# Optimization experiments

Measured on AMD Instinct MI355X. Metric: run time of the kernel, lower is better.

Reference implementation:

```python
import jax, jax.numpy as jnp
import numpy as np

R = 4096          # proposals per image
D = 4096          # fc7 feature dim (VGG16)
C = 20            # foreground classes (VOC); logits have C+1 with background
IMG_W, IMG_H = 1216.0, 800.0
SCORE_THRESH = 0.05
NMS_THRESH = 0.5
TOPK = 100


def setup_inputs() -> dict:
    key = jax.random.key(0)
    k1, k2, k3, k4, k5 = jax.random.split(key, 5)
    x = jax.random.normal(k1, (R, D), dtype=jnp.float32)
    # build valid xyxy boxes inside the image
    xy = jax.random.uniform(k2, (R, 2)) * jnp.array([IMG_W * 0.8, IMG_H * 0.8])
    wh = jax.random.uniform(k3, (R, 2)) * jnp.array([IMG_W * 0.4, IMG_H * 0.4]) + 8.0
    boxes = jnp.concatenate([xy, xy + wh], axis=1).astype(jnp.float32)
    W_cls = (jax.random.normal(k4, (D, C + 1)) * 0.01).astype(jnp.float32)
    W_det = (jax.random.normal(k5, (D, C + 1)) * 0.01).astype(jnp.float32)
    b_cls = jnp.zeros((C + 1,), jnp.float32)
    b_det = jnp.zeros((C + 1,), jnp.float32)
    return {"x": x, "boxes": boxes, "W_cls": W_cls, "b_cls": b_cls,
            "W_det": W_det, "b_det": b_det}


def _iou_matrix(b):
    # b: (R, 4) xyxy -> (R, R) IoU
    area = (b[:, 2] - b[:, 0]) * (b[:, 3] - b[:, 1])
    lt = jnp.maximum(b[:, None, :2], b[None, :, :2])
    rb = jnp.minimum(b[:, None, 2:], b[None, :, 2:])
    wh = jnp.clip(rb - lt, 0.0)
    inter = wh[..., 0] * wh[..., 1]
    return inter / (area[:, None] + area[None, :] - inter + 1e-9)


def _nms_per_class(sc, iou):
    # sc: (R,) scores for one class; iou: (R, R) shared IoU matrix.
    # Sequential greedy NMS over score-descending order; returns bool keep mask.
    n = sc.shape[0]
    order = jnp.argsort(-sc)

    def step(supp, oi):
        kept = (sc[oi] > SCORE_THRESH) & jnp.logical_not(supp[oi])
        supp = jnp.where(kept, supp | (iou[oi] > NMS_THRESH), supp)
        return supp, kept

    _, keep_sorted = jax.lax.scan(step, jnp.zeros((n,), bool), order)
    return jnp.zeros((n,), bool).at[order].set(keep_sorted)


def reference(x, boxes, W_cls, b_cls, W_det, b_det):
    # WSDDN two-stream head: class softmax x proposal softmax
    cls_logits = x @ W_cls + b_cls                      # (R, C+1)
    det_logits = x @ W_det + b_det                      # (R, C+1)
    scores = jax.nn.softmax(cls_logits, axis=1) * jax.nn.softmax(det_logits, axis=0)
    scores = scores[:, :-1]                             # drop background column (R, C)

    # clip boxes to image (Boxes.clip)
    b = jnp.stack([jnp.clip(boxes[:, 0], 0.0, IMG_W),
                   jnp.clip(boxes[:, 1], 0.0, IMG_H),
                   jnp.clip(boxes[:, 2], 0.0, IMG_W),
                   jnp.clip(boxes[:, 3], 0.0, IMG_H)], axis=1)

    iou = _iou_matrix(b)                                # (R, R)
    # per-class NMS (batched_nms with class-agnostic boxes == independent per-class NMS)
    keep = jax.vmap(lambda s: _nms_per_class(s, iou), in_axes=1, out_axes=1)(scores)  # (R, C)

    kept_scores = scores * keep.astype(scores.dtype)
    flat = kept_scores.reshape(-1)                      # (R*C,)
    top_vals, top_idx = jax.lax.top_k(flat, TOPK)
    top_prop = top_idx // C
    top_cls = top_idx % C
    top_boxes = b[top_prop]                             # (TOPK, 4)
    return top_vals, top_boxes, top_cls
```

## Files before the change

kernel.cpp:

```cpp
#include <hip/hip_runtime.h>
#include <math.h>

#define R_N 4096
#define D_N 4096
#define C_N 20
#define IMG_W_F 1216.0f
#define IMG_H_F 800.0f
#define SCORE_TH 0.05f
#define NMS_TH 0.5f
#define TOPK_N 100

#define WF_WORDS   (128 * 2 * 64 * 4)
#define DET_OFF    (WF_WORDS)
#define DET_WORDS  (R_N * 24)
#define CTRL_OFF   (DET_OFF + DET_WORDS)
#define CAND_R_OFF (CTRL_OFF + 64)
#define CAND_D_OFF (CAND_R_OFF + 640)
#define CAND_S_OFF (CAND_D_OFF + 640)

typedef short bf16x8 __attribute__((ext_vector_type(8)));
typedef float f32x4  __attribute__((ext_vector_type(4)));

__device__ __forceinline__ unsigned pk(float a, float b) {
  return __builtin_amdgcn_perm(__float_as_uint(a), __float_as_uint(b), 0x07060302u);
}
__device__ __forceinline__ float fexp(float x) { return __expf(x); }

__global__ __launch_bounds__(256) void wT_kernel(
    const float* __restrict__ Wd, uint4* __restrict__ Wfrag,
    float* __restrict__ ctrl) {
  const int e = blockIdx.x * 256 + threadIdx.x;
  const int l = e & 63;
  const int ct = (e >> 6) & 1;
  const int gs = e >> 7;
  const int c = ct * 16 + (l & 15);
  const int k0 = gs * 32 + (l >> 4) * 8;
  float w[8];
  if (c < 21) {
#pragma unroll
    for (int j = 0; j < 8; j++) w[j] = Wd[(size_t)(k0 + j) * 21 + c];
  } else {
#pragma unroll
    for (int j = 0; j < 8; j++) w[j] = 0.f;
  }
  uint4 v;
  v.x = pk(w[1], w[0]); v.y = pk(w[3], w[2]);
  v.z = pk(w[5], w[4]); v.w = pk(w[7], w[6]);
  Wfrag[(gs * 2 + ct) * 64 + l] = v;
  if (e < 64) ctrl[e] = 0.f;
}

__global__ __launch_bounds__(1024) void detgemm_kernel(
    const float* __restrict__ x, const uint4* __restrict__ Wfrag,
    float* __restrict__ detlog, float* __restrict__ dsum) {
  __shared__ float red[16 * 512];
  const int t = threadIdx.x;
  const int w = t >> 6, l = t & 63;
  const int r16 = l & 15, q = l >> 4;
  const int r0 = blockIdx.x * 16;

  const float* xrow = x + (size_t)(r0 + r16) * D_N + w * 256 + q * 8;

  float4 a[16];
#pragma unroll
  for (int s = 0; s < 8; s++) {
    a[2 * s]     = *(const float4*)(xrow + s * 32);
    a[2 * s + 1] = *(const float4*)(xrow + s * 32 + 4);
  }

  f32x4 acc0 = {0.f, 0.f, 0.f, 0.f};
  f32x4 acc1 = {0.f, 0.f, 0.f, 0.f};
#pragma unroll
  for (int s = 0; s < 8; s++) {
    const int gs = w * 8 + s;
    union { uint4 u; bf16x8 v; } b0, b1;
    b0.u = Wfrag[(gs * 2 + 0) * 64 + l];
    b1.u = Wfrag[(gs * 2 + 1) * 64 + l];
    union { bf16x8 v; unsigned u[4]; } af;
    af.u[0] = pk(a[2 * s].y,     a[2 * s].x);
    af.u[1] = pk(a[2 * s].w,     a[2 * s].z);
    af.u[2] = pk(a[2 * s + 1].y, a[2 * s + 1].x);
    af.u[3] = pk(a[2 * s + 1].w, a[2 * s + 1].z);
    acc0 = __builtin_amdgcn_mfma_f32_16x16x32_bf16(af.v, b0.v, acc0, 0, 0, 0);
    acc1 = __builtin_amdgcn_mfma_f32_16x16x32_bf16(af.v, b1.v, acc1, 0, 0, 0);
  }

  *(f32x4*)(&red[w * 512 + (0  + r16) * 16 + q * 4]) = acc0;
  *(f32x4*)(&red[w * 512 + (16 + r16) * 16 + q * 4]) = acc1;
  __syncthreads();
  if (t < 512) {
    float v = 0.f;
#pragma unroll
    for (int w2 = 0; w2 < 16; w2++) v += red[w2 * 512 + t];
    red[t] = v;
  }
  __syncthreads();
  if (t < 21) {
    float s = 0.f;
#pragma unroll
    for (int r = 0; r < 16; r++) {
      float v = red[t * 16 + r];
      detlog[(size_t)(r0 + r) * 24 + t] = v;
      s += fexp(v);
    }
    atomicAdd(&dsum[t], s);
  }
}

__device__ __forceinline__ void load_clip_box(const float* boxes, int r, float* b) {
  b[0] = fminf(fmaxf(boxes[r * 4 + 0], 0.f), IMG_W_F);
  b[1] = fminf(fmaxf(boxes[r * 4 + 1], 0.f), IMG_H_F);
  b[2] = fminf(fmaxf(boxes[r * 4 + 2], 0.f), IMG_W_F);
  b[3] = fminf(fmaxf(boxes[r * 4 + 3], 0.f), IMG_H_F);
}

__global__ __launch_bounds__(256) void finish_kernel(
    const float* __restrict__ x, const float* __restrict__ Wc,
    const float* __restrict__ b_cls, const float* __restrict__ detlog,
    const float* __restrict__ dsum, int* __restrict__ nc, int* __restrict__ done,
    int* __restrict__ cand_r, float* __restrict__ cand_d, float* __restrict__ cand_s,
    const float* __restrict__ boxes, float* __restrict__ out) {
  __shared__ float sd[20];
  __shared__ bool s_last;
  const int t = threadIdx.x;
  if (t < 20) sd[t] = dsum[t];
  __syncthreads();

  const int r = blockIdx.x * 256 + t;
  for (int c = 0; c < 20; c++) {
    float dsm = fexp(detlog[(size_t)r * 24 + c]) / sd[c];
    if (dsm > SCORE_TH) {
      int p = atomicAdd(&nc[c], 1);
      if (p < 32) { cand_r[c * 32 + p] = r; cand_d[c * 32 + p] = dsm; }
    }
  }
  __threadfence();
  __syncthreads();
  if (t == 0) s_last = (atomicAdd(done, 1) == 15);
  __syncthreads();
  if (!s_last) return;
  __threadfence();

  for (int slot = t; slot < 640; slot += 256) {
    const int c = slot >> 5, i = slot & 31;
    int n = nc[c]; if (n > 32) n = 32;
    if (i < n) {
      const int rr = cand_r[slot];
      float lg[21];
#pragma unroll
      for (int j = 0; j < 21; j++) lg[j] = b_cls[j];
      const float* xr = x + (size_t)rr * D_N;
      for (int k = 0; k < D_N; k++) {
        float xv = xr[k];
        const float* wr = Wc + (size_t)k * 21;
#pragma unroll
        for (int j = 0; j < 21; j++) lg[j] = fmaf(xv, wr[j], lg[j]);
      }
      float m = -1e30f;
#pragma unroll
      for (int j = 0; j < 21; j++) m = fmaxf(m, lg[j]);
      float s = 0.f;
#pragma unroll
      for (int j = 0; j < 21; j++) s += fexp(lg[j] - m);
      float p = fexp(lg[c] - m) / s;
      cand_s[slot] = p * cand_d[slot];
    }
  }
  __syncthreads();

  __shared__ int   s_kc;
  __shared__ int   s_ki[512];
  __shared__ float s_ks[512];
  __shared__ float sval[TOPK_N];
  __shared__ int   sidx[TOPK_N];
  if (t == 0) s_kc = 0;
  if (t < TOPK_N) { sval[t] = 0.f; sidx[t] = 0; }
  __syncthreads();

  if (t < 20) {
    const int c = t;
    int n = nc[c]; if (n > 32) n = 32;
    float s[32]; int rr[32]; int n2 = 0;
    for (int i = 0; i < n; i++) {
      float sc = cand_s[c * 32 + i];
      if (sc > SCORE_TH) { s[n2] = sc; rr[n2] = cand_r[c * 32 + i]; n2++; }
    }
    for (int i = 1; i < n2; i++) {
      float si = s[i]; int ri = rr[i];
      int j = i - 1;
      while (j >= 0 && (s[j] < si || (s[j] == si && rr[j] > ri))) {
        s[j + 1] = s[j]; rr[j + 1] = rr[j]; j--;
      }
      s[j + 1] = si; rr[j + 1] = ri;
    }
    unsigned supp = 0;
    for (int i = 0; i < n2; i++) {
      if (supp & (1u << i)) continue;
      int g = atomicAdd(&s_kc, 1);
      if (g < 512) { s_ki[g] = rr[i] * C_N + c; s_ks[g] = s[i]; }
      float bi[4]; load_clip_box(boxes, rr[i], bi);
      float ai = (bi[2] - bi[0]) * (bi[3] - bi[1]);
      for (int j = i + 1; j < n2; j++) {
        if (supp & (1u << j)) continue;
        float bj[4]; load_clip_box(boxes, rr[j], bj);
        float aj = (bj[2] - bj[0]) * (bj[3] - bj[1]);
        float lx = fmaxf(bi[0], bj[0]), ly = fmaxf(bi[1], bj[1]);
        float rx = fminf(bi[2], bj[2]), ry = fminf(bi[3], bj[3]);
        float wdt = fmaxf(rx - lx, 0.f), hgt = fmaxf(ry - ly, 0.f);
        float inter = wdt * hgt;
        float iou = inter / (ai + aj - inter + 1e-9f);
        if (iou > NMS_TH) supp |= (1u << j);
      }
    }
  }
  __syncthreads();

  int m = s_kc; if (m > 512) m = 512;
  for (int i = t; i < m; i += 256) {
    float si = s_ks[i]; int xi = s_ki[i];
    int rank = 0;
    for (int j = 0; j < m; j++) {
      float sj = s_ks[j]; int xj = s_ki[j];
      if (sj > si || (sj == si && xj < xi)) rank++;
    }
    if (rank < TOPK_N) { sval[rank] = si; sidx[rank] = xi; }
  }
  __syncthreads();
  if (t == 0) {
    int f = m < TOPK_N ? m : TOPK_N;
    int cur = 0;
    for (int slot = f; slot < TOPK_N; slot++) {
      for (;;) {
        bool member = false;
        for (int j = 0; j < m; j++)
          if (s_ki[j] == cur) { member = true; break; }
        if (!member) break;
        cur++;
      }
      sval[slot] = 0.f;
      sidx[slot] = cur;
      cur++;
    }
  }
  __syncthreads();
  if (t < TOPK_N) {
    int idx = sidx[t];
    int prop = idx / C_N;
    int cls = idx - prop * C_N;
    float b[4]; load_clip_box(boxes, prop, b);
    out[t] = sval[t];
    out[TOPK_N + t * 4 + 0] = b[0];
    out[TOPK_N + t * 4 + 1] = b[1];
    out[TOPK_N + t * 4 + 2] = b[2];
    out[TOPK_N + t * 4 + 3] = b[3];
    out[TOPK_N * 5 + t] = (float)cls;
  }
}

extern "C" void kernel_launch(void* const* d_in, const int* in_sizes, int n_in,
                              void* d_out, int out_size, void* d_ws, size_t ws_size,
                              hipStream_t stream) {
  const float* x     = (const float*)d_in[0];
  const float* boxes = (const float*)d_in[1];
  const float* W_cls = (const float*)d_in[2];
  const float* b_cls = (const float*)d_in[3];
  const float* W_det = (const float*)d_in[4];

  float* out = (float*)d_out;
  float* ws = (float*)d_ws;
  uint4* Wfrag    = (uint4*)ws;
  float* detlog   = ws + DET_OFF;
  float* dsum     = ws + CTRL_OFF;
  int*   nc       = (int*)(ws + CTRL_OFF) + 24;
  int*   done     = (int*)(ws + CTRL_OFF) + 44;
  int*   cand_r   = (int*)(ws + CAND_R_OFF);
  float* cand_d   = ws + CAND_D_OFF;
  float* cand_s   = ws + CAND_S_OFF;

  wT_kernel     <<<64,  256,  0, stream>>>(W_det, Wfrag, dsum);
  detgemm_kernel<<<256, 1024, 0, stream>>>(x, Wfrag, detlog, dsum);
  finish_kernel <<<16,  256,  0, stream>>>(x, W_cls, b_cls, detlog, dsum,
                                           nc, done, cand_r, cand_d, cand_s,
                                           boxes, out);
}
```

Measured before the change: 122.3 us.

## Fuse weight prep, det GEMM and finish into one kernel with last-block tail

```diff
diff --git a/kernel.cpp b/kernel.cpp
--- a/kernel.cpp
+++ b/kernel.cpp
@@ -10,57 +10,37 @@
 #define NMS_TH 0.5f
 #define TOPK_N 100
 
-#define WF_WORDS   (128 * 2 * 64 * 4)
-#define DET_OFF    (WF_WORDS)
-#define DET_WORDS  (R_N * 24)
-#define CTRL_OFF   (DET_OFF + DET_WORDS)
-#define CAND_R_OFF (CTRL_OFF + 64)
-#define CAND_D_OFF (CAND_R_OFF + 640)
-#define CAND_S_OFF (CAND_D_OFF + 640)
-
 typedef short bf16x8 __attribute__((ext_vector_type(8)));
 typedef float f32x4  __attribute__((ext_vector_type(4)));
+
+__device__ int g_done;
 
 __device__ __forceinline__ unsigned pk(float a, float b) {
   return __builtin_amdgcn_perm(__float_as_uint(a), __float_as_uint(b), 0x07060302u);
 }
 __device__ __forceinline__ float fexp(float x) { return __expf(x); }
 
-__global__ __launch_bounds__(256) void wT_kernel(
-    const float* __restrict__ Wd, uint4* __restrict__ Wfrag,
-    float* __restrict__ ctrl) {
-  const int e = blockIdx.x * 256 + threadIdx.x;
-  const int l = e & 63;
-  const int ct = (e >> 6) & 1;
-  const int gs = e >> 7;
-  const int c = ct * 16 + (l & 15);
-  const int k0 = gs * 32 + (l >> 4) * 8;
-  float w[8];
-  if (c < 21) {
-#pragma unroll
-    for (int j = 0; j < 8; j++) w[j] = Wd[(size_t)(k0 + j) * 21 + c];
-  } else {
-#pragma unroll
-    for (int j = 0; j < 8; j++) w[j] = 0.f;
-  }
-  uint4 v;
-  v.x = pk(w[1], w[0]); v.y = pk(w[3], w[2]);
-  v.z = pk(w[5], w[4]); v.w = pk(w[7], w[6]);
-  Wfrag[(gs * 2 + ct) * 64 + l] = v;
-  if (e < 64) ctrl[e] = 0.f;
+__device__ __forceinline__ void load_clip_box(const float* boxes, int r, float* b) {
+  b[0] = fminf(fmaxf(boxes[r * 4 + 0], 0.f), IMG_W_F);
+  b[1] = fminf(fmaxf(boxes[r * 4 + 1], 0.f), IMG_H_F);
+  b[2] = fminf(fmaxf(boxes[r * 4 + 2], 0.f), IMG_W_F);
+  b[3] = fminf(fmaxf(boxes[r * 4 + 3], 0.f), IMG_H_F);
 }
 
-__global__ __launch_bounds__(1024) void detgemm_kernel(
-    const float* __restrict__ x, const uint4* __restrict__ Wfrag,
-    float* __restrict__ detlog, float* __restrict__ dsum) {
-  __shared__ float red[16 * 512];
+__global__ __launch_bounds__(1024) void fused_kernel(
+    const float* __restrict__ x, const float* __restrict__ Wd,
+    const float* __restrict__ Wc, const float* __restrict__ b_cls,
+    const float* __restrict__ boxes,
+    float* __restrict__ detlog, float* __restrict__ out) {
+  __shared__ float smem[10752];
+  __shared__ int s_lastf;
+
   const int t = threadIdx.x;
   const int w = t >> 6, l = t & 63;
   const int r16 = l & 15, q = l >> 4;
   const int r0 = blockIdx.x * 16;
 
   const float* xrow = x + (size_t)(r0 + r16) * D_N + w * 256 + q * 8;
-
   float4 a[16];
 #pragma unroll
   for (int s = 0; s < 8; s++) {
@@ -68,15 +48,36 @@
     a[2 * s + 1] = *(const float4*)(xrow + s * 32 + 4);
   }
 
+  float* wb = smem + w * 672;
+  const int c0  = l & 15;
+  const bool v1 = (c0 < 5);
+  const int cc1 = v1 ? (16 + c0) : 0;
+  const int rb  = q * 8;
+
   f32x4 acc0 = {0.f, 0.f, 0.f, 0.f};
   f32x4 acc1 = {0.f, 0.f, 0.f, 0.f};
 #pragma unroll
   for (int s = 0; s < 8; s++) {
-    const int gs = w * 8 + s;
-    union { uint4 u; bf16x8 v; } b0, b1;
-    b0.u = Wfrag[(gs * 2 + 0) * 64 + l];
-    b1.u = Wfrag[(gs * 2 + 1) * 64 + l];
-    union { bf16x8 v; unsigned u[4]; } af;
+    const float* p = Wd + (size_t)((w * 256 + s * 32) * 21);
+    float4 w0 = *(const float4*)(p + 4 * l);
+    float4 w1 = *(const float4*)(p + 4 * l + 256);
+    *(float4*)(wb + 4 * l)       = w0;
+    *(float4*)(wb + 4 * l + 256) = w1;
+    if (l < 40) {
+      float4 w2 = *(const float4*)(p + 4 * l + 512);
+      *(float4*)(wb + 4 * l + 512) = w2;
+    }
+    union { bf16x8 v; unsigned u[4]; } b0, b1, af;
+#pragma unroll
+    for (int jj = 0; jj < 4; jj++) {
+      float e0 = wb[(rb + 2 * jj)     * 21 + c0];
+      float e1 = wb[(rb + 2 * jj + 1) * 21 + c0];
+      b0.u[jj] = pk(e1, e0);
+      float f0 = wb[(rb + 2 * jj)     * 21 + cc1];
+      float f1 = wb[(rb + 2 * jj + 1) * 21 + cc1];
+      unsigned uu = pk(f1, f0);
+      b1.u[jj] = v1 ? uu : 0u;
+    }
     af.u[0] = pk(a[2 * s].y,     a[2 * s].x);
     af.u[1] = pk(a[2 * s].w,     a[2 * s].z);
     af.u[2] = pk(a[2 * s + 1].y, a[2 * s + 1].x);
@@ -85,6 +86,8 @@
     acc1 = __builtin_amdgcn_mfma_f32_16x16x32_bf16(af.v, b1.v, acc1, 0, 0, 0);
   }
 
+  __syncthreads();
+  float* red = smem;
   *(f32x4*)(&red[w * 512 + (0  + r16) * 16 + q * 4]) = acc0;
   *(f32x4*)(&red[w * 512 + (16 + r16) * 16 + q * 4]) = acc1;
   __syncthreads();
@@ -96,54 +99,89 @@
   }
   __syncthreads();
   if (t < 21) {
-    float s = 0.f;
-#pragma unroll
-    for (int r = 0; r < 16; r++) {
-      float v = red[t * 16 + r];
-      detlog[(size_t)(r0 + r) * 24 + t] = v;
-      s += fexp(v);
-    }
-    atomicAdd(&dsum[t], s);
-  }
-}
-
-__device__ __forceinline__ void load_clip_box(const float* boxes, int r, float* b) {
-  b[0] = fminf(fmaxf(boxes[r * 4 + 0], 0.f), IMG_W_F);
-  b[1] = fminf(fmaxf(boxes[r * 4 + 1], 0.f), IMG_H_F);
-  b[2] = fminf(fmaxf(boxes[r * 4 + 2], 0.f), IMG_W_F);
-  b[3] = fminf(fmaxf(boxes[r * 4 + 3], 0.f), IMG_H_F);
-}
-
-__global__ __launch_bounds__(256) void finish_kernel(
-    const float* __restrict__ x, const float* __restrict__ Wc,
-    const float* __restrict__ b_cls, const float* __restrict__ detlog,
-    const float* __restrict__ dsum, int* __restrict__ nc, int* __restrict__ done,
-    int* __restrict__ cand_r, float* __restrict__ cand_d, float* __restrict__ cand_s,
-    const float* __restrict__ boxes, float* __restrict__ out) {
-  __shared__ float sd[20];
-  __shared__ bool s_last;
-  const int t = threadIdx.x;
-  if (t < 20) sd[t] = dsum[t];
-  __syncthreads();
-
-  const int r = blockIdx.x * 256 + t;
+#pragma unroll
+    for (int r = 0; r < 16; r++)
+      detlog[(size_t)(r0 + r) * 24 + t] = red[t * 16 + r];
+  }
+
+  __threadfence();
+  __syncthreads();
+  if (t == 0) s_lastf = (atomicAdd(&g_done, 1) == 255) ? 1 : 0;
+  __syncthreads();
+  if (!s_lastf) return;
+  __threadfence();
+
+  float* sd     = smem;
+  int*   nc_l   = (int*)(smem + 32);
+  int*   cand_r = (int*)(smem + 64);
+  float* cand_d = smem + 704;
+  float* cand_s = smem + 1344;
+  int*   s_ki   = (int*)(smem + 1984);
+  float* s_ks   = smem + 2496;
+  float* sval   = smem + 3008;
+  int*   sidx   = (int*)(smem + 3108);
+  float* wred   = smem + 3208;
+  int*   s_kc   = (int*)(smem + 3528);
+
+  float ps[20];
+#pragma unroll
+  for (int c = 0; c < 20; c++) ps[c] = 0.f;
+  for (int rr = t; rr < R_N; rr += 1024) {
+    const float* dp = detlog + (size_t)rr * 24;
+    union { float4 v[5]; float f[20]; } u;
+    u.v[0] = *(const float4*)(dp + 0);
+    u.v[1] = *(const float4*)(dp + 4);
+    u.v[2] = *(const float4*)(dp + 8);
+    u.v[3] = *(const float4*)(dp + 12);
+    u.v[4] = *(const float4*)(dp + 16);
+#pragma unroll
+    for (int c = 0; c < 20; c++) ps[c] += fexp(u.f[c]);
+  }
+#pragma unroll
   for (int c = 0; c < 20; c++) {
-    float dsm = fexp(detlog[(size_t)r * 24 + c]) / sd[c];
-    if (dsm > SCORE_TH) {
-      int p = atomicAdd(&nc[c], 1);
-      if (p < 32) { cand_r[c * 32 + p] = r; cand_d[c * 32 + p] = dsm; }
-    }
-  }
-  __threadfence();
-  __syncthreads();
-  if (t == 0) s_last = (atomicAdd(done, 1) == 15);
-  __syncthreads();
-  if (!s_last) return;
-  __threadfence();
-
-  for (int slot = t; slot < 640; slot += 256) {
+    float v = ps[c];
+#pragma unroll
+    for (int off = 32; off; off >>= 1) v += __shfl_xor(v, off, 64);
+    ps[c] = v;
+  }
+  if (l == 0) {
+#pragma unroll
+    for (int c = 0; c < 20; c++) wred[w * 20 + c] = ps[c];
+  }
+  __syncthreads();
+  if (t < 20) {
+    float v = 0.f;
+#pragma unroll
+    for (int w2 = 0; w2 < 16; w2++) v += wred[w2 * 20 + t];
+    sd[t] = v;
+    nc_l[t] = 0;
+  }
+  if (t == 0) *s_kc = 0;
+  if (t < TOPK_N) { sval[t] = 0.f; sidx[t] = 0; }
+  __syncthreads();
+
+  for (int rr = t; rr < R_N; rr += 1024) {
+    const float* dp = detlog + (size_t)rr * 24;
+    union { float4 v[5]; float f[20]; } u;
+    u.v[0] = *(const float4*)(dp + 0);
+    u.v[1] = *(const float4*)(dp + 4);
+    u.v[2] = *(const float4*)(dp + 8);
+    u.v[3] = *(const float4*)(dp + 12);
+    u.v[4] = *(const float4*)(dp + 16);
+#pragma unroll
+    for (int c = 0; c < 20; c++) {
+      float dsm = fexp(u.f[c]) / sd[c];
+      if (dsm > SCORE_TH) {
+        int p = atomicAdd(&nc_l[c], 1);
+        if (p < 32) { cand_r[c * 32 + p] = rr; cand_d[c * 32 + p] = dsm; }
+      }
+    }
+  }
+  __syncthreads();
+
+  for (int slot = t; slot < 640; slot += 1024) {
     const int c = slot >> 5, i = slot & 31;
-    int n = nc[c]; if (n > 32) n = 32;
+    int n = nc_l[c]; if (n > 32) n = 32;
     if (i < n) {
       const int rr = cand_r[slot];
       float lg[21];
@@ -168,18 +206,9 @@
   }
   __syncthreads();
 
-  __shared__ int   s_kc;
-  __shared__ int   s_ki[512];
-  __shared__ float s_ks[512];
-  __shared__ float sval[TOPK_N];
-  __shared__ int   sidx[TOPK_N];
-  if (t == 0) s_kc = 0;
-  if (t < TOPK_N) { sval[t] = 0.f; sidx[t] = 0; }
-  __syncthreads();
-
   if (t < 20) {
     const int c = t;
-    int n = nc[c]; if (n > 32) n = 32;
+    int n = nc_l[c]; if (n > 32) n = 32;
     float s[32]; int rr[32]; int n2 = 0;
     for (int i = 0; i < n; i++) {
       float sc = cand_s[c * 32 + i];
@@ -196,7 +225,7 @@
     unsigned supp = 0;
     for (int i = 0; i < n2; i++) {
       if (supp & (1u << i)) continue;
-      int g = atomicAdd(&s_kc, 1);
+      int g = atomicAdd(s_kc, 1);
       if (g < 512) { s_ki[g] = rr[i] * C_N + c; s_ks[g] = s[i]; }
       float bi[4]; load_clip_box(boxes, rr[i], bi);
       float ai = (bi[2] - bi[0]) * (bi[3] - bi[1]);
@@ -215,8 +244,8 @@
   }
   __syncthreads();
 
-  int m = s_kc; if (m > 512) m = 512;
-  for (int i = t; i < m; i += 256) {
+  int m = *s_kc; if (m > 512) m = 512;
+  for (int i = t; i < m; i += 1024) {
     float si = s_ks[i]; int xi = s_ki[i];
     int rank = 0;
     for (int j = 0; j < m; j++) {
@@ -255,6 +284,7 @@
     out[TOPK_N + t * 4 + 3] = b[3];
     out[TOPK_N * 5 + t] = (float)cls;
   }
+  if (t == 0) g_done = 0;
 }
 
 extern "C" void kernel_launch(void* const* d_in, const int* in_sizes, int n_in,
@@ -266,20 +296,8 @@
   const float* b_cls = (const float*)d_in[3];
   const float* W_det = (const float*)d_in[4];
 
-  float* out = (float*)d_out;
-  float* ws = (float*)d_ws;
-  uint4* Wfrag    = (uint4*)ws;
-  float* detlog   = ws + DET_OFF;
-  float* dsum     = ws + CTRL_OFF;
-  int*   nc       = (int*)(ws + CTRL_OFF) + 24;
-  int*   done     = (int*)(ws + CTRL_OFF) + 44;
-  int*   cand_r   = (int*)(ws + CAND_R_OFF);
-  float* cand_d   = ws + CAND_D_OFF;
-  float* cand_s   = ws + CAND_S_OFF;
-
-  wT_kernel     <<<64,  256,  0, stream>>>(W_det, Wfrag, dsum);
-  detgemm_kernel<<<256, 1024, 0, stream>>>(x, Wfrag, detlog, dsum);
-  finish_kernel <<<16,  256,  0, stream>>>(x, W_cls, b_cls, detlog, dsum,
-                                           nc, done, cand_r, cand_d, cand_s,
-                                           boxes, out);
+  float* out    = (float*)d_out;
+  float* detlog = (float*)d_ws;
+
+  fused_kernel<<<256, 1024, 0, stream>>>(x, W_det, W_cls, b_cls, boxes, detlog, out);
 }
```

After: 196.7 us. 1.61x slower.

## Split det GEMM over K halves and compute det softmax sums in single finish block

Applied to the files above, without the earlier changes.

```diff
diff --git a/kernel.cpp b/kernel.cpp
--- a/kernel.cpp
+++ b/kernel.cpp
@@ -12,11 +12,6 @@
 
 #define WF_WORDS   (128 * 2 * 64 * 4)
 #define DET_OFF    (WF_WORDS)
-#define DET_WORDS  (R_N * 24)
-#define CTRL_OFF   (DET_OFF + DET_WORDS)
-#define CAND_R_OFF (CTRL_OFF + 64)
-#define CAND_D_OFF (CAND_R_OFF + 640)
-#define CAND_S_OFF (CAND_D_OFF + 640)
 
 typedef short bf16x8 __attribute__((ext_vector_type(8)));
 typedef float f32x4  __attribute__((ext_vector_type(4)));
@@ -26,9 +21,16 @@
 }
 __device__ __forceinline__ float fexp(float x) { return __expf(x); }
 
+__device__ __forceinline__ void load_clip_box(const float* boxes, int r, float* b) {
+  b[0] = fminf(fmaxf(boxes[r * 4 + 0], 0.f), IMG_W_F);
+  b[1] = fminf(fmaxf(boxes[r * 4 + 1], 0.f), IMG_H_F);
+  b[2] = fminf(fmaxf(boxes[r * 4 + 2], 0.f), IMG_W_F);
+  b[3] = fminf(fmaxf(boxes[r * 4 + 3], 0.f), IMG_H_F);
+}
+
 __global__ __launch_bounds__(256) void wT_kernel(
     const float* __restrict__ Wd, uint4* __restrict__ Wfrag,
-    float* __restrict__ ctrl) {
+    float* __restrict__ detlog) {
   const int e = blockIdx.x * 256 + threadIdx.x;
   const int l = e & 63;
   const int ct = (e >> 6) & 1;
@@ -47,23 +49,26 @@
   v.x = pk(w[1], w[0]); v.y = pk(w[3], w[2]);
   v.z = pk(w[5], w[4]); v.w = pk(w[7], w[6]);
   Wfrag[(gs * 2 + ct) * 64 + l] = v;
-  if (e < 64) ctrl[e] = 0.f;
+#pragma unroll
+  for (int i = e; i < R_N * 24; i += 16384) detlog[i] = 0.f;
 }
 
 __global__ __launch_bounds__(1024) void detgemm_kernel(
     const float* __restrict__ x, const uint4* __restrict__ Wfrag,
-    float* __restrict__ detlog, float* __restrict__ dsum) {
+    float* __restrict__ detlog) {
   __shared__ float red[16 * 512];
   const int t = threadIdx.x;
   const int w = t >> 6, l = t & 63;
   const int r16 = l & 15, q = l >> 4;
-  const int r0 = blockIdx.x * 16;
-
-  const float* xrow = x + (size_t)(r0 + r16) * D_N + w * 256 + q * 8;
-
-  float4 a[16];
-#pragma unroll
-  for (int s = 0; s < 8; s++) {
+  const int rblk = blockIdx.x >> 1;
+  const int kb   = blockIdx.x & 1;
+  const int r0 = rblk * 16;
+
+  const float* xrow = x + (size_t)(r0 + r16) * D_N + kb * 2048 + w * 128 + q * 8;
+
+  float4 a[8];
+#pragma unroll
+  for (int s = 0; s < 4; s++) {
     a[2 * s]     = *(const float4*)(xrow + s * 32);
     a[2 * s + 1] = *(const float4*)(xrow + s * 32 + 4);
   }
@@ -71,8 +76,8 @@
   f32x4 acc0 = {0.f, 0.f, 0.f, 0.f};
   f32x4 acc1 = {0.f, 0.f, 0.f, 0.f};
 #pragma unroll
-  for (int s = 0; s < 8; s++) {
-    const int gs = w * 8 + s;
+  for (int s = 0; s < 4; s++) {
+    const int gs = kb * 64 + w * 4 + s;
     union { uint4 u; bf16x8 v; } b0, b1;
     b0.u = Wfrag[(gs * 2 + 0) * 64 + l];
     b1.u = Wfrag[(gs * 2 + 1) * 64 + l];
@@ -88,60 +93,89 @@
   *(f32x4*)(&red[w * 512 + (0  + r16) * 16 + q * 4]) = acc0;
   *(f32x4*)(&red[w * 512 + (16 + r16) * 16 + q * 4]) = acc1;
   __syncthreads();
-  if (t < 512) {
+  if (t < 336) {
     float v = 0.f;
 #pragma unroll
     for (int w2 = 0; w2 < 16; w2++) v += red[w2 * 512 + t];
-    red[t] = v;
-  }
-  __syncthreads();
-  if (t < 21) {
-    float s = 0.f;
-#pragma unroll
-    for (int r = 0; r < 16; r++) {
-      float v = red[t * 16 + r];
-      detlog[(size_t)(r0 + r) * 24 + t] = v;
-      s += fexp(v);
-    }
-    atomicAdd(&dsum[t], s);
-  }
-}
-
-__device__ __forceinline__ void load_clip_box(const float* boxes, int r, float* b) {
-  b[0] = fminf(fmaxf(boxes[r * 4 + 0], 0.f), IMG_W_F);
-  b[1] = fminf(fmaxf(boxes[r * 4 + 1], 0.f), IMG_H_F);
-  b[2] = fminf(fmaxf(boxes[r * 4 + 2], 0.f), IMG_W_F);
-  b[3] = fminf(fmaxf(boxes[r * 4 + 3], 0.f), IMG_H_F);
-}
-
-__global__ __launch_bounds__(256) void finish_kernel(
+    atomicAdd(&detlog[(size_t)(r0 + (t & 15)) * 24 + (t >> 4)], v);
+  }
+}
+
+__global__ __launch_bounds__(1024) void finish_kernel(
     const float* __restrict__ x, const float* __restrict__ Wc,
     const float* __restrict__ b_cls, const float* __restrict__ detlog,
-    const float* __restrict__ dsum, int* __restrict__ nc, int* __restrict__ done,
-    int* __restrict__ cand_r, float* __restrict__ cand_d, float* __restrict__ cand_s,
     const float* __restrict__ boxes, float* __restrict__ out) {
   __shared__ float sd[20];
-  __shared__ bool s_last;
+  __shared__ float wred[16 * 20];
+  __shared__ int   nc[20];
+  __shared__ int   cand_r[640];
+  __shared__ float cand_d[640];
+  __shared__ float cand_s[640];
+  __shared__ int   s_ki[512];
+  __shared__ float s_ks[512];
+  __shared__ float sval[TOPK_N];
+  __shared__ int   sidx[TOPK_N];
+  __shared__ int   s_kc;
   const int t = threadIdx.x;
-  if (t < 20) sd[t] = dsum[t];
-  __syncthreads();
-
-  const int r = blockIdx.x * 256 + t;
+  const int w = t >> 6, l = t & 63;
+
+  float ps[20];
+#pragma unroll
+  for (int c = 0; c < 20; c++) ps[c] = 0.f;
+  for (int rr = t; rr < R_N; rr += 1024) {
+    const float* dp = detlog + (size_t)rr * 24;
+    union { float4 v[5]; float f[20]; } u;
+    u.v[0] = *(const float4*)(dp + 0);
+    u.v[1] = *(const float4*)(dp + 4);
+    u.v[2] = *(const float4*)(dp + 8);
+    u.v[3] = *(const float4*)(dp + 12);
+    u.v[4] = *(const float4*)(dp + 16);
+#pragma unroll
+    for (int c = 0; c < 20; c++) ps[c] += fexp(u.f[c]);
+  }
+#pragma unroll
   for (int c = 0; c < 20; c++) {
-    float dsm = fexp(detlog[(size_t)r * 24 + c]) / sd[c];
-    if (dsm > SCORE_TH) {
-      int p = atomicAdd(&nc[c], 1);
-      if (p < 32) { cand_r[c * 32 + p] = r; cand_d[c * 32 + p] = dsm; }
-    }
-  }
-  __threadfence();
-  __syncthreads();
-  if (t == 0) s_last = (atomicAdd(done, 1) == 15);
-  __syncthreads();
-  if (!s_last) return;
-  __threadfence();
-
-  for (int slot = t; slot < 640; slot += 256) {
+    float v = ps[c];
+#pragma unroll
+    for (int off = 32; off; off >>= 1) v += __shfl_xor(v, off, 64);
+    ps[c] = v;
+  }
+  if (l == 0) {
+#pragma unroll
+    for (int c = 0; c < 20; c++) wred[w * 20 + c] = ps[c];
+  }
+  __syncthreads();
+  if (t < 20) {
+    float v = 0.f;
+#pragma unroll
+    for (int w2 = 0; w2 < 16; w2++) v += wred[w2 * 20 + t];
+    sd[t] = v;
+    nc[t] = 0;
+  }
+  if (t == 0) s_kc = 0;
+  if (t < TOPK_N) { sval[t] = 0.f; sidx[t] = 0; }
+  __syncthreads();
+
+  for (int rr = t; rr < R_N; rr += 1024) {
+    const float* dp = detlog + (size_t)rr * 24;
+    union { float4 v[5]; float f[20]; } u;
+    u.v[0] = *(const float4*)(dp + 0);
+    u.v[1] = *(const float4*)(dp + 4);
+    u.v[2] = *(const float4*)(dp + 8);
+    u.v[3] = *(const float4*)(dp + 12);
+    u.v[4] = *(const float4*)(dp + 16);
+#pragma unroll
+    for (int c = 0; c < 20; c++) {
+      float dsm = fexp(u.f[c]) / sd[c];
+      if (dsm > SCORE_TH) {
+        int p = atomicAdd(&nc[c], 1);
+        if (p < 32) { cand_r[c * 32 + p] = rr; cand_d[c * 32 + p] = dsm; }
+      }
+    }
+  }
+  __syncthreads();
+
+  for (int slot = t; slot < 640; slot += 1024) {
     const int c = slot >> 5, i = slot & 31;
     int n = nc[c]; if (n > 32) n = 32;
     if (i < n) {
@@ -166,15 +200,6 @@
       cand_s[slot] = p * cand_d[slot];
     }
   }
-  __syncthreads();
-
-  __shared__ int   s_kc;
-  __shared__ int   s_ki[512];
-  __shared__ float s_ks[512];
-  __shared__ float sval[TOPK_N];
-  __shared__ int   sidx[TOPK_N];
-  if (t == 0) s_kc = 0;
-  if (t < TOPK_N) { sval[t] = 0.f; sidx[t] = 0; }
   __syncthreads();
 
   if (t < 20) {
@@ -216,7 +241,7 @@
   __syncthreads();
 
   int m = s_kc; if (m > 512) m = 512;
-  for (int i = t; i < m; i += 256) {
+  for (int i = t; i < m; i += 1024) {
     float si = s_ks[i]; int xi = s_ki[i];
     int rank = 0;
     for (int j = 0; j < m; j++) {
@@ -268,18 +293,10 @@
 
   float* out = (float*)d_out;
   float* ws = (float*)d_ws;
-  uint4* Wfrag    = (uint4*)ws;
-  float* detlog   = ws + DET_OFF;
-  float* dsum     = ws + CTRL_OFF;
-  int*   nc       = (int*)(ws + CTRL_OFF) + 24;
-  int*   done     = (int*)(ws + CTRL_OFF) + 44;
-  int*   cand_r   = (int*)(ws + CAND_R_OFF);
-  float* cand_d   = ws + CAND_D_OFF;
-  float* cand_s   = ws + CAND_S_OFF;
-
-  wT_kernel     <<<64,  256,  0, stream>>>(W_det, Wfrag, dsum);
-  detgemm_kernel<<<256, 1024, 0, stream>>>(x, Wfrag, detlog, dsum);
-  finish_kernel <<<16,  256,  0, stream>>>(x, W_cls, b_cls, detlog, dsum,
-                                           nc, done, cand_r, cand_d, cand_s,
-                                           boxes, out);
-}
+  uint4* Wfrag  = (uint4*)ws;
+  float* detlog = ws + DET_OFF;
+
+  wT_kernel     <<<64,  256,  0, stream>>>(W_det, Wfrag, detlog);
+  detgemm_kernel<<<512, 1024, 0, stream>>>(x, Wfrag, detlog);
+  finish_kernel <<<1,   1024, 0, stream>>>(x, W_cls, b_cls, detlog, boxes, out);
+}
```

New measurement: 134.8 us. 10.2% more time.

## Fuse finish kernel into detection GEMM using a grid-wide spin barrier

Applied to the files above, without the earlier changes.

```diff
diff --git a/kernel.cpp b/kernel.cpp
--- a/kernel.cpp
+++ b/kernel.cpp
@@ -11,12 +11,9 @@
 #define TOPK_N 100
 
 #define WF_WORDS   (128 * 2 * 64 * 4)
-#define DET_OFF    (WF_WORDS)
-#define DET_WORDS  (R_N * 24)
-#define CTRL_OFF   (DET_OFF + DET_WORDS)
+#define CTRL_OFF   (WF_WORDS)
 #define CAND_R_OFF (CTRL_OFF + 64)
 #define CAND_D_OFF (CAND_R_OFF + 640)
-#define CAND_S_OFF (CAND_D_OFF + 640)
 
 typedef short bf16x8 __attribute__((ext_vector_type(8)));
 typedef float f32x4  __attribute__((ext_vector_type(4)));
@@ -26,9 +23,16 @@
 }
 __device__ __forceinline__ float fexp(float x) { return __expf(x); }
 
+__device__ __forceinline__ void load_clip_box(const float* boxes, int r, float* b) {
+  b[0] = fminf(fmaxf(boxes[r * 4 + 0], 0.f), IMG_W_F);
+  b[1] = fminf(fmaxf(boxes[r * 4 + 1], 0.f), IMG_H_F);
+  b[2] = fminf(fmaxf(boxes[r * 4 + 2], 0.f), IMG_W_F);
+  b[3] = fminf(fmaxf(boxes[r * 4 + 3], 0.f), IMG_H_F);
+}
+
 __global__ __launch_bounds__(256) void wT_kernel(
     const float* __restrict__ Wd, uint4* __restrict__ Wfrag,
-    float* __restrict__ ctrl) {
+    int* __restrict__ ctrl) {
   const int e = blockIdx.x * 256 + threadIdx.x;
   const int l = e & 63;
   const int ct = (e >> 6) & 1;
@@ -47,20 +51,28 @@
   v.x = pk(w[1], w[0]); v.y = pk(w[3], w[2]);
   v.z = pk(w[5], w[4]); v.w = pk(w[7], w[6]);
   Wfrag[(gs * 2 + ct) * 64 + l] = v;
-  if (e < 64) ctrl[e] = 0.f;
+  if (e < 42) ctrl[e] = 0;
 }
 
 __global__ __launch_bounds__(1024) void detgemm_kernel(
     const float* __restrict__ x, const uint4* __restrict__ Wfrag,
-    float* __restrict__ detlog, float* __restrict__ dsum) {
+    float* __restrict__ dsum, int* __restrict__ nc,
+    int* __restrict__ done1, int* __restrict__ done2,
+    int* __restrict__ cand_r, float* __restrict__ cand_d,
+    const float* __restrict__ Wc, const float* __restrict__ b_cls,
+    const float* __restrict__ boxes, float* __restrict__ out) {
   __shared__ float red[16 * 512];
+  __shared__ float ex[320];
+  __shared__ float sd[20];
+  __shared__ int   snc[20];
+  __shared__ int   s_last, s_total;
+
   const int t = threadIdx.x;
   const int w = t >> 6, l = t & 63;
   const int r16 = l & 15, q = l >> 4;
   const int r0 = blockIdx.x * 16;
 
   const float* xrow = x + (size_t)(r0 + r16) * D_N + w * 256 + q * 8;
-
   float4 a[16];
 #pragma unroll
   for (int s = 0; s < 8; s++) {
@@ -95,57 +107,81 @@
     red[t] = v;
   }
   __syncthreads();
-  if (t < 21) {
+  if (t < 320) ex[t] = fexp(red[t]);
+  __syncthreads();
+  if (t < 20) {
     float s = 0.f;
 #pragma unroll
-    for (int r = 0; r < 16; r++) {
-      float v = red[t * 16 + r];
-      detlog[(size_t)(r0 + r) * 24 + t] = v;
-      s += fexp(v);
-    }
+    for (int r = 0; r < 16; r++) s += ex[t * 16 + r];
     atomicAdd(&dsum[t], s);
   }
-}
-
-__device__ __forceinline__ void load_clip_box(const float* boxes, int r, float* b) {
-  b[0] = fminf(fmaxf(boxes[r * 4 + 0], 0.f), IMG_W_F);
-  b[1] = fminf(fmaxf(boxes[r * 4 + 1], 0.f), IMG_H_F);
-  b[2] = fminf(fmaxf(boxes[r * 4 + 2], 0.f), IMG_W_F);
-  b[3] = fminf(fmaxf(boxes[r * 4 + 3], 0.f), IMG_H_F);
-}
-
-__global__ __launch_bounds__(256) void finish_kernel(
-    const float* __restrict__ x, const float* __restrict__ Wc,
-    const float* __restrict__ b_cls, const float* __restrict__ detlog,
-    const float* __restrict__ dsum, int* __restrict__ nc, int* __restrict__ done,
-    int* __restrict__ cand_r, float* __restrict__ cand_d, float* __restrict__ cand_s,
-    const float* __restrict__ boxes, float* __restrict__ out) {
-  __shared__ float sd[20];
-  __shared__ bool s_last;
-  const int t = threadIdx.x;
-  if (t < 20) sd[t] = dsum[t];
-  __syncthreads();
-
-  const int r = blockIdx.x * 256 + t;
-  for (int c = 0; c < 20; c++) {
-    float dsm = fexp(detlog[(size_t)r * 24 + c]) / sd[c];
+  __syncthreads();
+
+  if (t == 0) {
+    atomicAdd(done1, 1);
+    while (atomicAdd(done1, 0) < 256) __builtin_amdgcn_s_sleep(8);
+  }
+  __syncthreads();
+  if (t < 20) sd[t] = atomicAdd(&dsum[t], 0.0f);
+  __syncthreads();
+
+  if (t < 320) {
+    const int c = t >> 4, r = t & 15;
+    float dsm = ex[t] / sd[c];
     if (dsm > SCORE_TH) {
       int p = atomicAdd(&nc[c], 1);
-      if (p < 32) { cand_r[c * 32 + p] = r; cand_d[c * 32 + p] = dsm; }
-    }
-  }
-  __threadfence();
-  __syncthreads();
-  if (t == 0) s_last = (atomicAdd(done, 1) == 15);
+      if (p < 32) {
+        atomicExch(&cand_r[c * 32 + p], r0 + r);
+        atomicExch(&cand_d[c * 32 + p], dsm);
+      }
+    }
+  }
+  __syncthreads();
+  if (t == 0) s_last = (atomicAdd(done2, 1) == 255) ? 1 : 0;
   __syncthreads();
   if (!s_last) return;
-  __threadfence();
-
-  for (int slot = t; slot < 640; slot += 256) {
+
+  if (t < 20) snc[t] = atomicAdd(&nc[t], 0);
+  __syncthreads();
+  if (t == 0) {
+    int tot = 0;
+#pragma unroll
+    for (int c = 0; c < 20; c++) tot += (snc[c] > 32 ? 32 : snc[c]);
+    s_total = tot;
+  }
+  __syncthreads();
+
+  if (s_total == 0) {
+    if (t < TOPK_N) {
+      int prop = t / C_N;
+      int cls = t - prop * C_N;
+      float b[4]; load_clip_box(boxes, prop, b);
+      out[t] = 0.f;
+      out[TOPK_N + t * 4 + 0] = b[0];
+      out[TOPK_N + t * 4 + 1] = b[1];
+      out[TOPK_N + t * 4 + 2] = b[2];
+      out[TOPK_N + t * 4 + 3] = b[3];
+      out[TOPK_N * 5 + t] = (float)cls;
+    }
+    return;
+  }
+
+  float* cand_s = red;
+  int*   s_ki   = (int*)(red + 640);
+  float* s_ks   = red + 1152;
+  float* sval   = red + 1664;
+  int*   sidx   = (int*)(red + 1764);
+  int*   s_kc   = (int*)(red + 1864);
+
+  if (t == 0) *s_kc = 0;
+  if (t < TOPK_N) { sval[t] = 0.f; sidx[t] = 0; }
+  __syncthreads();
+
+  for (int slot = t; slot < 640; slot += 1024) {
     const int c = slot >> 5, i = slot & 31;
-    int n = nc[c]; if (n > 32) n = 32;
+    int n = snc[c]; if (n > 32) n = 32;
     if (i < n) {
-      const int rr = cand_r[slot];
+      const int rr = atomicAdd(&cand_r[slot], 0);
       float lg[21];
 #pragma unroll
       for (int j = 0; j < 21; j++) lg[j] = b_cls[j];
@@ -163,27 +199,18 @@
 #pragma unroll
       for (int j = 0; j < 21; j++) s += fexp(lg[j] - m);
       float p = fexp(lg[c] - m) / s;
-      cand_s[slot] = p * cand_d[slot];
-    }
-  }
-  __syncthreads();
-
-  __shared__ int   s_kc;
-  __shared__ int   s_ki[512];
-  __shared__ float s_ks[512];
-  __shared__ float sval[TOPK_N];
-  __shared__ int   sidx[TOPK_N];
-  if (t == 0) s_kc = 0;
-  if (t < TOPK_N) { sval[t] = 0.f; sidx[t] = 0; }
+      cand_s[slot] = p * atomicAdd(&cand_d[slot], 0.0f);
+    }
+  }
   __syncthreads();
 
   if (t < 20) {
     const int c = t;
-    int n = nc[c]; if (n > 32) n = 32;
+    int n = snc[c]; if (n > 32) n = 32;
     float s[32]; int rr[32]; int n2 = 0;
     for (int i = 0; i < n; i++) {
       float sc = cand_s[c * 32 + i];
-      if (sc > SCORE_TH) { s[n2] = sc; rr[n2] = cand_r[c * 32 + i]; n2++; }
+      if (sc > SCORE_TH) { s[n2] = sc; rr[n2] = atomicAdd(&cand_r[c * 32 + i], 0); n2++; }
     }
     for (int i = 1; i < n2; i++) {
       float si = s[i]; int ri = rr[i];
@@ -196,7 +223,7 @@
     unsigned supp = 0;
     for (int i = 0; i < n2; i++) {
       if (supp & (1u << i)) continue;
-      int g = atomicAdd(&s_kc, 1);
+      int g = atomicAdd(s_kc, 1);
       if (g < 512) { s_ki[g] = rr[i] * C_N + c; s_ks[g] = s[i]; }
       float bi[4]; load_clip_box(boxes, rr[i], bi);
       float ai = (bi[2] - bi[0]) * (bi[3] - bi[1]);
@@ -215,8 +242,8 @@
   }
   __syncthreads();
 
-  int m = s_kc; if (m > 512) m = 512;
-  for (int i = t; i < m; i += 256) {
+  int m = *s_kc; if (m > 512) m = 512;
+  for (int i = t; i < m; i += 1024) {
     float si = s_ks[i]; int xi = s_ki[i];
     int rank = 0;
     for (int j = 0; j < m; j++) {
@@ -268,18 +295,15 @@
 
   float* out = (float*)d_out;
   float* ws = (float*)d_ws;
-  uint4* Wfrag    = (uint4*)ws;
-  float* detlog   = ws + DET_OFF;
-  float* dsum     = ws + CTRL_OFF;
-  int*   nc       = (int*)(ws + CTRL_OFF) + 24;
-  int*   done     = (int*)(ws + CTRL_OFF) + 44;
-  int*   cand_r   = (int*)(ws + CAND_R_OFF);
-  float* cand_d   = ws + CAND_D_OFF;
-  float* cand_s   = ws + CAND_S_OFF;
-
-  wT_kernel     <<<64,  256,  0, stream>>>(W_det, Wfrag, dsum);
-  detgemm_kernel<<<256, 1024, 0, stream>>>(x, Wfrag, detlog, dsum);
-  finish_kernel <<<16,  256,  0, stream>>>(x, W_cls, b_cls, detlog, dsum,
-                                           nc, done, cand_r, cand_d, cand_s,
-                                           boxes, out);
-}
+  uint4* Wfrag  = (uint4*)ws;
+  float* dsum   = ws + CTRL_OFF;
+  int*   nc     = (int*)(ws + CTRL_OFF) + 20;
+  int*   done1  = (int*)(ws + CTRL_OFF) + 40;
+  int*   done2  = (int*)(ws + CTRL_OFF) + 41;
+  int*   cand_r = (int*)(ws + CAND_R_OFF);
+  float* cand_d = ws + CAND_D_OFF;
+
+  wT_kernel     <<<64,  256,  0, stream>>>(W_det, Wfrag, (int*)(ws + CTRL_OFF));
+  detgemm_kernel<<<256, 1024, 0, stream>>>(x, Wfrag, dsum, nc, done1, done2,
+                                           cand_r, cand_d, W_cls, b_cls, boxes, out);
+}
```

Result: no change. 120.3 us (-1.6%).
